# Optimization experiments

Measured on AMD Instinct MI355X. Metric: run time of the kernel, lower is better.

Reference implementation:

```python
import jax, jax.numpy as jnp
import numpy as np

B, S, VD, MD = 32, 2048, 512, 512
AD = max(VD, MD)


def setup_inputs() -> dict:
    key = jax.random.key(0)
    k1, k2, k3, k4, k5, k6 = jax.random.split(key, 6)
    query = jax.random.normal(k1, (B, VD), dtype=jnp.float32)
    keys = jax.random.normal(k2, (B, S, MD), dtype=jnp.float32)
    mask = jax.random.randint(k3, (B, S), 0, 2).astype(jnp.bool_)
    # torch Linear weight layout: [out, in]
    W1 = jax.random.normal(k4, (AD, VD), dtype=jnp.float32) * (1.0 / np.sqrt(VD))
    W2 = jax.random.normal(k5, (AD, MD), dtype=jnp.float32) * (1.0 / np.sqrt(MD))
    v = jax.random.normal(k6, (AD,), dtype=jnp.float32) * (1.0 / np.sqrt(AD))
    return {"query": query, "keys": keys, "mask": mask, "W1": W1, "W2": W2, "v": v}


def reference(query, keys, mask, W1, W2, v):
    # w1_query: [B, 1, AD]; w2_keys: [B, S, AD]
    w1_query = jnp.einsum('bd,ad->ba', query, W1)[:, None, :]
    w2_keys = jnp.einsum('bsd,ad->bsa', keys, W2)
    combined = jnp.tanh(w1_query + w2_keys)            # [B, S, AD]
    scores = jnp.einsum('bsa,a->bs', combined, v)      # [B, S]
    scores = jnp.where(mask, scores, -jnp.inf)
    attn_weights = jax.nn.softmax(scores, axis=-1)
    return attn_weights
```

## Files before the change

### kernel.cpp

```cpp
#include <hip/hip_runtime.h>
#include <math.h>

#define BB 32
#define SS 2048
#define DD 512
#define AD 512

#define BM 128
#define BN 128
#define BK 64

typedef __bf16 bf16;
typedef __attribute__((ext_vector_type(8))) __bf16 bf16x8;
typedef __attribute__((ext_vector_type(4))) __bf16 bf16x4;
typedef __attribute__((ext_vector_type(4))) float floatx4;

__device__ inline void async16(const void* g, void* l) {
    __builtin_amdgcn_global_load_lds(
        (const __attribute__((address_space(1))) unsigned int*)g,
        (__attribute__((address_space(3))) unsigned int*)l, 16, 0, 0);
}

#define NW8 (AD * DD / 8)
#define NCV (NW8 / 256)
__global__ void prep_kernel(const float* __restrict__ W2,
                            bf16* __restrict__ W2b,
                            const unsigned char* __restrict__ m8,
                            int* __restrict__ flag,
                            const float* __restrict__ query,
                            const float* __restrict__ W1,
                            float* __restrict__ w1q,
                            int* __restrict__ cnt,
                            int* __restrict__ idxb) {
    const int bid = blockIdx.x;
    if (bid < NCV) {
        int j = threadIdx.x + bid * 256;
        const float4* s4 = (const float4*)W2 + (size_t)j * 2;
        float4 x = s4[0], y = s4[1];
        bf16x8 o;
        o[0] = (bf16)x.x; o[1] = (bf16)x.y; o[2] = (bf16)x.z; o[3] = (bf16)x.w;
        o[4] = (bf16)y.x; o[5] = (bf16)y.y; o[6] = (bf16)y.z; o[7] = (bf16)y.w;
        *(bf16x8*)(W2b + (size_t)j * 8) = o;
    } else if (bid < NCV + 64) {
        int t = threadIdx.x + (bid - NCV) * 256;
        int any = 0;
        for (int i = t; i < BB * SS; i += 64 * 256)
            if ((i & 3) && m8[i]) any = 1;
        if (__any(any)) {
            if ((threadIdx.x & 63) == 0) atomicOr(flag, 1);
        }
    } else if (bid < NCV + 64 + 4096) {
        int id = bid - NCV - 64;
        int b = id >> 7;
        int a = (id & 127) * 4 + (threadIdx.x >> 6);
        int lane = threadIdx.x & 63;
        const float4* q4 = (const float4*)(query + (size_t)b * DD) + lane * 2;
        const float4* w4 = (const float4*)(W1 + (size_t)a * DD) + lane * 2;
        float4 qa = q4[0], qb = q4[1];
        float4 wa = w4[0], wb = w4[1];
        float acc = qa.x * wa.x + qa.y * wa.y + qa.z * wa.z + qa.w * wa.w
                  + qb.x * wb.x + qb.y * wb.y + qb.z * wb.z + qb.w * wb.w;
#pragma unroll
        for (int off = 32; off > 0; off >>= 1) acc += __shfl_down(acc, off);
        if (lane == 0) w1q[(size_t)b * AD + a] = acc;
    } else {
        const int b = bid - NCV - 64 - 4096;
        const int t = threadIdx.x;
        const int lane = t & 63, wid = t >> 6;
        __shared__ int s_base;
        __shared__ int wsum[4];
        __shared__ int s_bytes;
        if (t == 0) { s_base = 0; s_bytes = 0; }
        __syncthreads();
        {
            const unsigned* mu = (const unsigned*)m8;
            unsigned pr = (mu[t] | mu[t + 256]) & 0xFFFFFF00u;
            if (pr) atomicOr(&s_bytes, 1);
        }
        __syncthreads();
        const int bytes = s_bytes;
        const int* m32 = (const int*)m8;
#pragma unroll 1
        for (int c = 0; c < 8; ++c) {
            int s = c * 256 + t;
            int mv = bytes ? (int)m8[(size_t)b * SS + s]
                           : m32[(size_t)b * SS + s];
            unsigned long long ball = __ballot(mv != 0);
            int rank = __popcll(ball & ((1ull << lane) - 1ull));
            if (lane == 0) wsum[wid] = __popcll(ball);
            __syncthreads();
            int woff = s_base;
            for (int j = 0; j < wid; ++j) woff += wsum[j];
            if (mv) idxb[(size_t)b * SS + woff + rank] = s;
            __syncthreads();
            if (t == 0) s_base += wsum[0] + wsum[1] + wsum[2] + wsum[3];
            __syncthreads();
        }
        if (t == 0) cnt[b] = s_base;
    }
}

__global__ __launch_bounds__(256, 3)
void gemm_scores_mfma(const float* __restrict__ keys,
                      const bf16* __restrict__ W2b,
                      const float* __restrict__ w1q,
                      const float* __restrict__ v,
                      const int* __restrict__ cnt,
                      const int* __restrict__ idxb,
                      float* __restrict__ partial) {
    __shared__ float a_lds[BM * BK];
    __shared__ bf16  b_lds[BN * BK];
    __shared__ int   idx_lds[BM];

    const int t    = threadIdx.x;
    const int lane = t & 63;
    const int w    = t >> 6;
    const int ml   = lane & 15;
    const int kg   = lane >> 4;

    const int lin    = blockIdx.x;
    const int x8     = lin & 7;
    const int hi     = lin >> 3;
    const int a_tile = hi & 3;
    const int kt     = x8 + ((hi >> 2) << 3);
    const int b      = kt >> 4;
    const int s0     = (kt & 15) * BM;
    const int a0     = a_tile * BN;

    const int cntb = cnt[b];
    if (s0 >= cntb) return;

    const int m_off = (w & 1) * 64;
    const int n_off = (w >> 1) * 64;

    const float* Akeys = keys + (size_t)b * SS * DD;
    const bf16*  Bblk  = W2b + (size_t)a0 * DD;

    if (t < BM) {
        int p = s0 + t;
        idx_lds[t] = idxb[(size_t)b * SS + (p < cntb ? p : cntb - 1)];
    }
    __syncthreads();

    int arow[8];
#pragma unroll
    for (int i = 0; i < 8; ++i) arow[i] = idx_lds[(t + 256 * i) >> 4];

    floatx4 acc[4][4];
#pragma unroll
    for (int mi = 0; mi < 4; ++mi)
#pragma unroll
        for (int ni = 0; ni < 4; ++ni)
            acc[mi][ni] = (floatx4)(0.f);

    const int NCHUNK = DD / BK;
    for (int c = 0; c < NCHUNK; ++c) {
        const int d0 = c * BK;
        __syncthreads();
#pragma unroll
        for (int i = 0; i < 8; ++i) {
            int g = t + 256 * i;
            int r = g >> 4, cc = g & 15, cs = cc ^ (r & 15);
            async16(Akeys + (size_t)arow[i] * DD + d0 + cs * 4,
                    &a_lds[(256 * i + 64 * w) * 4]);
        }
#pragma unroll
        for (int i = 0; i < 4; ++i) {
            int g = t + 256 * i;
            int r = g >> 3, cc = g & 7, cs = cc ^ (r & 7);
            async16(Bblk + (size_t)r * DD + d0 + cs * 8,
                    &b_lds[(256 * i + 64 * w) * 8]);
        }
        __syncthreads();

#pragma unroll
        for (int ks = 0; ks < 2; ++ks) {
            bf16x8 af[4], bfr[4];
#pragma unroll
            for (int mi = 0; mi < 4; ++mi) {
                int R  = m_off + mi * 16 + ml;
                int gB = 8 * ks + 2 * kg;
                float4 lo = *(const float4*)&a_lds[R * BK + ((gB    ) ^ (R & 15)) * 4];
                float4 hi4 = *(const float4*)&a_lds[R * BK + ((gB + 1) ^ (R & 15)) * 4];
                bf16x8 f;
                f[0] = (bf16)lo.x;  f[1] = (bf16)lo.y;
                f[2] = (bf16)lo.z;  f[3] = (bf16)lo.w;
                f[4] = (bf16)hi4.x; f[5] = (bf16)hi4.y;
                f[6] = (bf16)hi4.z; f[7] = (bf16)hi4.w;
                af[mi] = f;
            }
#pragma unroll
            for (int ni = 0; ni < 4; ++ni) {
                int R = n_off + ni * 16 + ml;
                int pos = (ks * 4 + kg) ^ (R & 7);
                bfr[ni] = *(const bf16x8*)&b_lds[R * BK + pos * 8];
            }
#pragma unroll
            for (int mi = 0; mi < 4; ++mi)
#pragma unroll
                for (int ni = 0; ni < 4; ++ni)
                    acc[mi][ni] = __builtin_amdgcn_mfma_f32_16x16x32_bf16(
                        af[mi], bfr[ni], acc[mi][ni], 0, 0, 0);
        }
    }

    float w1qa[4], va[4];
#pragma unroll
    for (int ni = 0; ni < 4; ++ni) {
        int a = a0 + n_off + ni * 16 + ml;
        w1qa[ni] = w1q[(size_t)b * AD + a];
        va[ni]   = v[a];
    }
    const int slot = a_tile * 2 + (w >> 1);
#pragma unroll
    for (int mi = 0; mi < 4; ++mi) {
#pragma unroll
        for (int reg = 0; reg < 4; ++reg) {
            float p = 0.f;
#pragma unroll
            for (int ni = 0; ni < 4; ++ni) {
                float x = acc[mi][ni][reg] + w1qa[ni];
                float th = 1.f - 2.f / (1.f + __expf(2.f * x));
                p = fmaf(th, va[ni], p);
            }
            p += __shfl_xor(p, 1);
            p += __shfl_xor(p, 2);
            p += __shfl_xor(p, 4);
            p += __shfl_xor(p, 8);
            int row = m_off + mi * 16 + kg * 4 + reg;
            if (ml == 0 && s0 + row < cntb) {
                int os = idx_lds[row];
                partial[((size_t)b * SS + os) * 8 + slot] = p;
            }
        }
    }
}

#define FBK 32
#define FLDK (FBK + 8)
__global__ __launch_bounds__(256, 2)
void gemm_scores_fallback(const float* __restrict__ keys,
                          const float* __restrict__ W2,
                          const float* __restrict__ w1q,
                          const float* __restrict__ v,
                          float* __restrict__ partial) {
    __shared__ bf16 a_lds[BM][FLDK];
    __shared__ bf16 b_lds[BN][FLDK];
    __shared__ float s_red[BM];

    const int t    = threadIdx.x;
    const int lane = t & 63;
    const int w    = t >> 6;
    const int ml   = lane & 15;
    const int kg   = lane >> 4;
    const int b    = blockIdx.z;
    const int s0   = blockIdx.x * BM;
    const int a0   = blockIdx.y * BN;
    const int m_off = (w & 1) * 64;
    const int n_off = (w >> 1) * 64;

    const float* Ablk = keys + ((size_t)b * SS + s0) * DD;
    const float* Bblk = W2 + (size_t)a0 * DD;

    if (t < BM) s_red[t] = 0.f;

    floatx4 acc[4][4];
#pragma unroll
    for (int mi = 0; mi < 4; ++mi)
#pragma unroll
        for (int ni = 0; ni < 4; ++ni)
            acc[mi][ni] = (floatx4)(0.f);

    float4 ga[4], gb[4];
#pragma unroll
    for (int i = 0; i < 4; ++i) {
        int idx = t + 256 * i;
        int r = idx >> 3, c = idx & 7;
        ga[i] = *(const float4*)(Ablk + (size_t)r * DD + c * 4);
        gb[i] = *(const float4*)(Bblk + (size_t)r * DD + c * 4);
    }

    for (int chunk = 0; chunk < DD / FBK; ++chunk) {
        __syncthreads();
#pragma unroll
        for (int i = 0; i < 4; ++i) {
            int idx = t + 256 * i;
            int r = idx >> 3, c = idx & 7;
            bf16x4 pa, pb;
            pa[0] = (bf16)ga[i].x; pa[1] = (bf16)ga[i].y;
            pa[2] = (bf16)ga[i].z; pa[3] = (bf16)ga[i].w;
            pb[0] = (bf16)gb[i].x; pb[1] = (bf16)gb[i].y;
            pb[2] = (bf16)gb[i].z; pb[3] = (bf16)gb[i].w;
            *(bf16x4*)&a_lds[r][c * 4] = pa;
            *(bf16x4*)&b_lds[r][c * 4] = pb;
        }
        __syncthreads();
        if (chunk < DD / FBK - 1) {
            int d0 = (chunk + 1) * FBK;
#pragma unroll
            for (int i = 0; i < 4; ++i) {
                int idx = t + 256 * i;
                int r = idx >> 3, c = idx & 7;
                ga[i] = *(const float4*)(Ablk + (size_t)r * DD + d0 + c * 4);
                gb[i] = *(const float4*)(Bblk + (size_t)r * DD + d0 + c * 4);
            }
        }
        bf16x8 af[4], bfr[4];
#pragma unroll
        for (int mi = 0; mi < 4; ++mi)
            af[mi] = *(const bf16x8*)&a_lds[m_off + mi * 16 + ml][kg * 8];
#pragma unroll
        for (int ni = 0; ni < 4; ++ni)
            bfr[ni] = *(const bf16x8*)&b_lds[n_off + ni * 16 + ml][kg * 8];
#pragma unroll
        for (int mi = 0; mi < 4; ++mi)
#pragma unroll
            for (int ni = 0; ni < 4; ++ni)
                acc[mi][ni] = __builtin_amdgcn_mfma_f32_16x16x32_bf16(
                    af[mi], bfr[ni], acc[mi][ni], 0, 0, 0);
    }

    float w1qa[4], va[4];
#pragma unroll
    for (int ni = 0; ni < 4; ++ni) {
        int a = a0 + n_off + ni * 16 + ml;
        w1qa[ni] = w1q[(size_t)b * AD + a];
        va[ni]   = v[a];
    }
#pragma unroll
    for (int mi = 0; mi < 4; ++mi) {
#pragma unroll
        for (int reg = 0; reg < 4; ++reg) {
            float p = 0.f;
#pragma unroll
            for (int ni = 0; ni < 4; ++ni) {
                float x = acc[mi][ni][reg] + w1qa[ni];
                float th = 1.f - 2.f / (1.f + __expf(2.f * x));
                p = fmaf(th, va[ni], p);
            }
            p += __shfl_xor(p, 1);
            p += __shfl_xor(p, 2);
            p += __shfl_xor(p, 4);
            p += __shfl_xor(p, 8);
            if (ml == 0)
                atomicAdd(&s_red[m_off + mi * 16 + kg * 4 + reg], p);
        }
    }
    __syncthreads();
    if (t < BM)
        partial[(((size_t)b * SS) + s0 + t) * 8 + blockIdx.y * 2] = s_red[t];
}

__global__ void softmax_kernel(const float* __restrict__ partial,
                               const int* __restrict__ mask_i32,
                               const unsigned char* __restrict__ mask_u8,
                               const int* __restrict__ flag,
                               float* __restrict__ out) {
    const int b = blockIdx.x;
    const int t = threadIdx.x;
    __shared__ float rmax[4], rsum[4];
    const int wid = t >> 6, lane = t & 63;

    float sv[8]; int mv[8];
    const int bytes = (*flag != 0);
#pragma unroll
    for (int k = 0; k < 8; ++k) {
        int i = t + 256 * k;
        const float4* p4 = (const float4*)(partial + ((size_t)b * SS + i) * 8);
        float4 pa = p4[0], pb = p4[1];
        sv[k] = ((pa.x + pa.y) + (pa.z + pa.w)) + ((pb.x + pb.y) + (pb.z + pb.w));
        mv[k] = bytes ? (int)mask_u8[(size_t)b * SS + i]
                      : mask_i32[(size_t)b * SS + i];
    }

    float mx = -INFINITY;
#pragma unroll
    for (int k = 0; k < 8; ++k) mx = fmaxf(mx, mv[k] ? sv[k] : -INFINITY);
#pragma unroll
    for (int off = 32; off > 0; off >>= 1) mx = fmaxf(mx, __shfl_xor(mx, off));
    if (lane == 0) rmax[wid] = mx;
    __syncthreads();
    mx = fmaxf(fmaxf(rmax[0], rmax[1]), fmaxf(rmax[2], rmax[3]));

    float ev[8]; float sum = 0.f;
#pragma unroll
    for (int k = 0; k < 8; ++k) {
        ev[k] = mv[k] ? __expf(sv[k] - mx) : 0.f;
        sum += ev[k];
    }
#pragma unroll
    for (int off = 32; off > 0; off >>= 1) sum += __shfl_xor(sum, off);
    if (lane == 0) rsum[wid] = sum;
    __syncthreads();
    sum = (rsum[0] + rsum[1]) + (rsum[2] + rsum[3]);
    float inv = 1.f / sum;
#pragma unroll
    for (int k = 0; k < 8; ++k)
        out[(size_t)b * SS + t + 256 * k] = ev[k] * inv;
}

extern "C" void kernel_launch(void* const* d_in, const int* in_sizes, int n_in,
                              void* d_out, int out_size, void* d_ws, size_t ws_size,
                              hipStream_t stream) {
    const float* query = (const float*)d_in[0];
    const float* keys  = (const float*)d_in[1];
    const void*  mask  = d_in[2];
    const float* W1    = (const float*)d_in[3];
    const float* W2    = (const float*)d_in[4];
    const float* v     = (const float*)d_in[5];
    float* out = (float*)d_out;

    char* wsb = (char*)d_ws;
    int*   flag    = (int*)wsb;
    float* w1q     = (float*)(wsb + 256);
    float* partial = (float*)(wsb + 256 + 65536);
    bf16*  W2b     = (bf16*)(wsb + 256 + 65536 + 2097152);
    int*   cnt     = (int*)(wsb + 256 + 65536 + 2097152 + 524288);
    int*   idxb    = (int*)(wsb + 256 + 65536 + 2097152 + 524288 + 256);
    size_t need = 256 + 65536 + 2097152 + 524288 + 256
                + (size_t)BB * SS * sizeof(int);

    hipMemsetAsync(flag, 0, 4, stream);
    if (ws_size >= need) {
        prep_kernel<<<NCV + 64 + 4096 + 32, 256, 0, stream>>>(
            W2, W2b, (const unsigned char*)mask, flag, query, W1, w1q,
            cnt, idxb);
        gemm_scores_mfma<<<(SS / BM) * (AD / BN) * BB, 256, 0, stream>>>(
            keys, W2b, w1q, v, cnt, idxb, partial);
    } else {
        hipMemsetAsync(partial, 0, (size_t)BB * SS * 8 * 4, stream);
        prep_kernel<<<NCV + 64 + 4096, 256, 0, stream>>>(
            W2, (bf16*)(wsb + 256 + 65536 + 2097152),
            (const unsigned char*)mask, flag, query, W1, w1q,
            nullptr, nullptr);
        gemm_scores_fallback<<<dim3(SS / BM, AD / BN, BB), 256, 0, stream>>>(
            keys, W2, w1q, v, partial);
    }
    softmax_kernel<<<BB, 256, 0, stream>>>(partial, (const int*)mask,
                                           (const unsigned char*)mask, flag, out);
}
```

Baseline: 245.0 us.

## Fuse softmax into scores GEMM via last-block atomic counter per batch

```diff
diff --git a/kernel.cpp b/kernel.cpp
--- a/kernel.cpp
+++ b/kernel.cpp
@@ -107,10 +107,17 @@
                       const float* __restrict__ v,
                       const int* __restrict__ cnt,
                       const int* __restrict__ idxb,
-                      float* __restrict__ partial) {
+                      float* __restrict__ partial,
+                      const int* __restrict__ mask_i32,
+                      const unsigned char* __restrict__ mask_u8,
+                      const int* __restrict__ flag,
+                      int* __restrict__ bcnt,
+                      float* __restrict__ out) {
     __shared__ float a_lds[BM * BK];
     __shared__ bf16  b_lds[BN * BK];
     __shared__ int   idx_lds[BM];
+    __shared__ float rmax[4], rsum[4];
+    __shared__ int   s_last;
 
     const int t    = threadIdx.x;
     const int lane = t & 63;
@@ -234,6 +241,56 @@
             }
         }
     }
+
+    __threadfence();
+    if (t == 0) {
+        const int nact = 4 * ((cntb + BM - 1) / BM);
+        int old = atomicAdd(&bcnt[b], 1);
+        s_last = (old == nact - 1);
+    }
+    __syncthreads();
+    if (!s_last) return;
+    __threadfence();
+
+    {
+        const int wid = w;
+        const int bytes = (*flag != 0);
+        float sv[8]; int mv[8];
+#pragma unroll
+        for (int k = 0; k < 8; ++k) {
+            int i = t + 256 * k;
+            const float4* p4 = (const float4*)(partial + ((size_t)b * SS + i) * 8);
+            float4 pa = p4[0], pb = p4[1];
+            sv[k] = ((pa.x + pa.y) + (pa.z + pa.w)) + ((pb.x + pb.y) + (pb.z + pb.w));
+            mv[k] = bytes ? (int)mask_u8[(size_t)b * SS + i]
+                          : mask_i32[(size_t)b * SS + i];
+        }
+
+        float mx = -INFINITY;
+#pragma unroll
+        for (int k = 0; k < 8; ++k) mx = fmaxf(mx, mv[k] ? sv[k] : -INFINITY);
+#pragma unroll
+        for (int off = 32; off > 0; off >>= 1) mx = fmaxf(mx, __shfl_xor(mx, off));
+        if (lane == 0) rmax[wid] = mx;
+        __syncthreads();
+        mx = fmaxf(fmaxf(rmax[0], rmax[1]), fmaxf(rmax[2], rmax[3]));
+
+        float ev[8]; float sum = 0.f;
+#pragma unroll
+        for (int k = 0; k < 8; ++k) {
+            ev[k] = mv[k] ? __expf(sv[k] - mx) : 0.f;
+            sum += ev[k];
+        }
+#pragma unroll
+        for (int off = 32; off > 0; off >>= 1) sum += __shfl_xor(sum, off);
+        if (lane == 0) rsum[wid] = sum;
+        __syncthreads();
+        sum = (rsum[0] + rsum[1]) + (rsum[2] + rsum[3]);
+        float inv = 1.f / sum;
+#pragma unroll
+        for (int k = 0; k < 8; ++k)
+            out[(size_t)b * SS + t + 256 * k] = ev[k] * inv;
+    }
 }
 
 #define FBK 32
@@ -412,6 +469,7 @@
 
     char* wsb = (char*)d_ws;
     int*   flag    = (int*)wsb;
+    int*   bcnt    = (int*)(wsb + 64);
     float* w1q     = (float*)(wsb + 256);
     float* partial = (float*)(wsb + 256 + 65536);
     bf16*  W2b     = (bf16*)(wsb + 256 + 65536 + 2097152);
@@ -420,14 +478,16 @@
     size_t need = 256 + 65536 + 2097152 + 524288 + 256
                 + (size_t)BB * SS * sizeof(int);
 
-    hipMemsetAsync(flag, 0, 4, stream);
     if (ws_size >= need) {
+        hipMemsetAsync(wsb, 0, 256, stream);
         prep_kernel<<<NCV + 64 + 4096 + 32, 256, 0, stream>>>(
             W2, W2b, (const unsigned char*)mask, flag, query, W1, w1q,
             cnt, idxb);
         gemm_scores_mfma<<<(SS / BM) * (AD / BN) * BB, 256, 0, stream>>>(
-            keys, W2b, w1q, v, cnt, idxb, partial);
+            keys, W2b, w1q, v, cnt, idxb, partial,
+            (const int*)mask, (const unsigned char*)mask, flag, bcnt, out);
     } else {
+        hipMemsetAsync(wsb, 0, 256, stream);
         hipMemsetAsync(partial, 0, (size_t)BB * SS * 8 * 4, stream);
         prep_kernel<<<NCV + 64 + 4096, 256, 0, stream>>>(
             W2, (bf16*)(wsb + 256 + 65536 + 2097152),
@@ -435,7 +495,8 @@
             nullptr, nullptr);
         gemm_scores_fallback<<<dim3(SS / BM, AD / BN, BB), 256, 0, stream>>>(
             keys, W2, w1q, v, partial);
-    }
-    softmax_kernel<<<BB, 256, 0, stream>>>(partial, (const int*)mask,
-                                           (const unsigned char*)mask, flag, out);
+        softmax_kernel<<<BB, 256, 0, stream>>>(partial, (const int*)mask,
+                                               (const unsigned char*)mask,
+                                               flag, out);
+    }
 }
```

After: 520.3 us. 2.12x slower.
